# Kernel tuning notes

Measured on AMD Instinct MI355X. Metric: run time of the kernel, lower is better.

## Reference

```python
import jax, jax.numpy as jnp
import numpy as np

B, DIM, H, W = 512, 256, 14, 14
HEADS, KD, VD = 4, 16, 64  # key_dim=16, val_dim=attn_ratio*key_dim=64
RES = 14


def _bn(x, g, b, rm, rv, eps=1e-5):
    # eval-mode BatchNorm2d folded into per-channel affine
    s = g / jnp.sqrt(rv + eps)
    return x * s[None, :, None, None] + (b - rm * s)[None, :, None, None]


def setup_inputs() -> dict:
    key = jax.random.key(0)
    ks = jax.random.split(key, 6)
    # relative position bias index table: offset (|dy|,|dx|) -> flat index
    ii = np.arange(RES * RES)
    ry, rx = ii // RES, ii % RES
    dyo = np.abs(ry[:, None] - ry[None, :])
    dxo = np.abs(rx[:, None] - rx[None, :])
    bias_idxs = jnp.asarray(dyo * RES + dxo, dtype=jnp.int32)  # [196,196]
    QKV_OUT = 2 * KD + VD  # 96
    inp = {
        'x': jax.random.normal(ks[0], (B, DIM, H, W), jnp.float32),
        'qkv_w': jax.random.normal(ks[1], (HEADS, QKV_OUT, DIM // HEADS), jnp.float32) * 0.05,
        'qkv_g': jnp.ones((HEADS, QKV_OUT), jnp.float32),
        'qkv_b': jnp.zeros((HEADS, QKV_OUT), jnp.float32),
        'qkv_rm': jnp.zeros((HEADS, QKV_OUT), jnp.float32),
        'qkv_rv': jnp.ones((HEADS, QKV_OUT), jnp.float32),
        'dw_w': jax.random.normal(ks[2], (HEADS, KD, 1, 5, 5), jnp.float32) * 0.05,
        'dw_g': jnp.ones((HEADS, KD), jnp.float32),
        'dw_b': jnp.zeros((HEADS, KD), jnp.float32),
        'dw_rm': jnp.zeros((HEADS, KD), jnp.float32),
        'dw_rv': jnp.ones((HEADS, KD), jnp.float32),
        'proj_w': jax.random.normal(ks[3], (DIM, VD * HEADS), jnp.float32) * 0.05,
        'proj_g': jnp.ones((DIM,), jnp.float32),
        'proj_b': jnp.zeros((DIM,), jnp.float32),
        'proj_rm': jnp.zeros((DIM,), jnp.float32),
        'proj_rv': jnp.ones((DIM,), jnp.float32),
        'attn_biases': jax.random.normal(ks[4], (HEADS, RES * RES), jnp.float32) * 0.02,
        'bias_idxs': bias_idxs,
    }
    return inp


def reference(x, qkv_w, qkv_g, qkv_b, qkv_rm, qkv_rv,
              dw_w, dw_g, dw_b, dw_rm, dw_rv,
              proj_w, proj_g, proj_b, proj_rm, proj_rv,
              attn_biases, bias_idxs):
    Bc, C, Hc, Wc = x.shape
    N = Hc * Wc
    scale = KD ** -0.5
    bias = attn_biases[:, bias_idxs]  # [HEADS, N, N]
    chunks = jnp.split(x, HEADS, axis=1)  # per-head [B, dim//heads, H, W]
    feat = chunks[0]
    outs = []
    for h in range(HEADS):  # cascading residual -> inherently sequential over heads
        if h > 0:
            feat = feat + chunks[h]
        f = jnp.einsum('oc,bchw->bohw', qkv_w[h], feat)  # 1x1 conv
        f = _bn(f, qkv_g[h], qkv_b[h], qkv_rm[h], qkv_rv[h])
        q, k, v = f[:, :KD], f[:, KD:2 * KD], f[:, 2 * KD:]
        # 5x5 depthwise conv on q, padding 2
        q = jax.lax.conv_general_dilated(
            q, dw_w[h], window_strides=(1, 1), padding=[(2, 2), (2, 2)],
            dimension_numbers=('NCHW', 'OIHW', 'NCHW'), feature_group_count=KD)
        q = _bn(q, dw_g[h], dw_b[h], dw_rm[h], dw_rv[h])
        qf = q.reshape(Bc, KD, N) * scale
        kf = k.reshape(Bc, KD, N)
        vf = v.reshape(Bc, VD, N)
        attn = jnp.einsum('bdn,bdm->bnm', qf, kf) + bias[h]  # [B, N, N]
        attn = jax.nn.softmax(attn, axis=-1)
        feat = jnp.einsum('bdm,bnm->bdn', vf, attn).reshape(Bc, VD, Hc, Wc)
        outs.append(feat)
    y = jax.nn.relu(jnp.concatenate(outs, axis=1))  # [B, VD*HEADS, H, W]
    y = jnp.einsum('oc,bchw->bohw', proj_w, y)
    return _bn(y, proj_g, proj_b, proj_rm, proj_rv)
```

## Files before the change

### kernel.cpp

```cpp
#include <hip/hip_runtime.h>
#include <math.h>

#define BATCH 512
#define DIM 256
#define HEADS 4
#define KD 16
#define VD 64
#define NQ 196
#define CHW (DIM * NQ)

typedef __attribute__((ext_vector_type(8))) short short8;
typedef __attribute__((ext_vector_type(4))) float f32x4;

#define MFMA16(A, B, C) __builtin_amdgcn_mfma_f32_16x16x32_bf16((A), (B), (C), 0, 0, 0)

__device__ __forceinline__ unsigned short f2bf(float f) {
    unsigned int u = __float_as_uint(f);
    u += 0x7FFFu + ((u >> 16) & 1u);
    return (unsigned short)(u >> 16);
}
__device__ __forceinline__ float bf2f(unsigned short h) {
    return __uint_as_float(((unsigned int)h) << 16);
}

#define OFF_QC    0
#define OFF_P0    16640
#define OFF_P1    33280
#define OFF_QRAW  49920
#define OFF_KB1   63232
#define OFF_KB2   81152
#define OFF_VBH   99072
#define OFF_VBL   128768
#define OFF_DEN4  158464
#define OFF_SB    161792
#define OFF_TB    162176
#define OFF_DWS   162560
#define OFF_DWT   162624
#define SMEM_BYTES 162688

__global__ __launch_bounds__(256)
void prep_kernel(const float* __restrict__ attn_biases,
                 const int* __restrict__ bias_idxs,
                 const float* __restrict__ qkv_w,
                 const float* __restrict__ proj_w,
                 float* __restrict__ biasg,
                 unsigned short* __restrict__ whH,
                 unsigned short* __restrict__ whL,
                 unsigned short* __restrict__ pwH,
                 unsigned short* __restrict__ pwL) {
    int i = blockIdx.x * 256 + threadIdx.x;
    const int T1 = HEADS * NQ * NQ;
    const int T2 = HEADS * 96 * 64;
    const int T3 = DIM * DIM;
    if (i < T1) {
        int h = i / (NQ * NQ);
        int r = i - h * (NQ * NQ);
        biasg[i] = attn_biases[h * NQ + bias_idxs[r]];
    } else if (i < T1 + T2) {
        int j = i - T1;
        float v = qkv_w[j];
        unsigned short hh = f2bf(v);
        whH[j] = hh;
        whL[j] = f2bf(v - bf2f(hh));
    } else if (i < T1 + T2 + T3) {
        int j = i - T1 - T2;
        float v = proj_w[j];
        unsigned short hh = f2bf(v);
        pwH[j] = hh;
        pwL[j] = f2bf(v - bf2f(hh));
    }
}

__global__ __launch_bounds__(1024, 4)
void cascade_attn_kernel(const float* __restrict__ x,
                         const unsigned short* __restrict__ whH,
                         const unsigned short* __restrict__ whL,
                         const float* __restrict__ qkv_g,
                         const float* __restrict__ qkv_b,
                         const float* __restrict__ qkv_rm,
                         const float* __restrict__ qkv_rv,
                         const float* __restrict__ dw_w,
                         const float* __restrict__ dw_g,
                         const float* __restrict__ dw_b,
                         const float* __restrict__ dw_rm,
                         const float* __restrict__ dw_rv,
                         const float* __restrict__ biasg,
                         unsigned short* __restrict__ yrelu,
                         const unsigned short* __restrict__ pwH,
                         const unsigned short* __restrict__ pwL,
                         const float* __restrict__ pg,
                         const float* __restrict__ pb,
                         const float* __restrict__ prm,
                         const float* __restrict__ prv,
                         float* __restrict__ out) {
    extern __shared__ __align__(16) char smem[];
    unsigned short* featU = (unsigned short*)(smem + OFF_QC);
    unsigned short* qc    = (unsigned short*)(smem + OFF_QC);
    unsigned short* Pb0   = (unsigned short*)(smem + OFF_P0);
    unsigned short* Pb1   = (unsigned short*)(smem + OFF_P1);
    float*          qraw  = (float*)(smem + OFF_QRAW);
    unsigned short* kb1   = (unsigned short*)(smem + OFF_KB1);
    unsigned short* kb2   = (unsigned short*)(smem + OFF_KB2);
    unsigned short* vbH   = (unsigned short*)(smem + OFF_VBH);
    unsigned short* vbL   = (unsigned short*)(smem + OFF_VBL);
    float*          den4  = (float*)(smem + OFF_DEN4);
    float*          sbT   = (float*)(smem + OFF_SB);
    float*          tbT   = (float*)(smem + OFF_TB);
    float*          dwsT  = (float*)(smem + OFF_DWS);
    float*          dwtT  = (float*)(smem + OFF_DWT);

    const int b    = blockIdx.x;
    const int tid  = threadIdx.x;
    const int w    = tid >> 6;
    const int li   = tid & 15;
    const int quad = (tid >> 4) & 3;
    const int tn0  = tid % NQ;
    const int tc0  = tid / NQ;

    for (int t = tid; t < SMEM_BYTES / 4; t += 1024) ((unsigned int*)smem)[t] = 0u;
    __syncthreads();
    for (int t = tid; t < VD * NQ; t += 1024) {
        int n = t % NQ, c = t / NQ;
        featU[n * 72 + c] = f2bf(x[((size_t)b * DIM + c) * NQ + n]);
    }
    __syncthreads();

    for (int h = 0; h < HEADS; ++h) {
        if (tid < 96) {
            float s = qkv_g[h * 96 + tid] * rsqrtf(qkv_rv[h * 96 + tid] + 1e-5f);
            sbT[tid] = s;
            tbT[tid] = qkv_b[h * 96 + tid] - qkv_rm[h * 96 + tid] * s;
        } else if (tid < 112) {
            int c = tid - 96;
            float s = dw_g[h * 16 + c] * rsqrtf(dw_rv[h * 16 + c] + 1e-5f);
            dwsT[c] = s;
            dwtT[c] = dw_b[h * 16 + c] - dw_rm[h * 16 + c] * s;
        }
        __syncthreads();

        for (int T = w; T < 78; T += 16) {
            int ot = T / 13, nt = T - ot * 13;
            const size_t wb = ((size_t)h * 96 + ot * 16 + li) * 64;
            short8 ah0 = *(const short8*)(whH + wb + quad * 8);
            short8 al0 = *(const short8*)(whL + wb + quad * 8);
            short8 ah1 = *(const short8*)(whH + wb + 32 + quad * 8);
            short8 al1 = *(const short8*)(whL + wb + 32 + quad * 8);
            short8 b0 = *(const short8*)(featU + (nt * 16 + li) * 72 + quad * 8);
            short8 b1 = *(const short8*)(featU + (nt * 16 + li) * 72 + 32 + quad * 8);
            f32x4 acc = {0.f, 0.f, 0.f, 0.f};
            acc = MFMA16(ah0, b0, acc);
            acc = MFMA16(al0, b0, acc);
            acc = MFMA16(ah1, b1, acc);
            acc = MFMA16(al1, b1, acc);
            int n = nt * 16 + li;
            bool nok = (n < NQ);
            #pragma unroll
            for (int r = 0; r < 4; ++r) {
                int o = ot * 16 + quad * 4 + r;
                float val = acc[r] * sbT[o] + tbT[o];
                if (nok) {
                    if (o < 16) {
                        qraw[o * 208 + n] = val;
                    } else if (o < 32) {
                        int c = o - 16;
                        unsigned short hh = f2bf(val);
                        kb1[n * 40 + c] = hh;
                        kb1[n * 40 + 16 + c] = hh;
                        kb2[n * 40 + c] = f2bf(val - bf2f(hh));
                    } else {
                        int d = o - 32;
                        unsigned short hh = f2bf(val);
                        vbH[d * 232 + n] = hh;
                        vbL[d * 232 + n] = f2bf(val - bf2f(hh));
                    }
                }
            }
        }
        __syncthreads();

        {
            int n = tn0, c = tc0, py = tn0 / 14, px = tn0 - (tn0 / 14) * 14;
            for (int t = tid; t < KD * NQ; t += 1024) {
                const float* qr = qraw + c * 208;
                const float* wdc = dw_w + ((size_t)h * KD + c) * 25;
                float accv = 0.f;
                #pragma unroll
                for (int ky = 0; ky < 5; ++ky) {
                    int yy = py + ky - 2;
                    if (yy < 0 || yy >= 14) continue;
                    #pragma unroll
                    for (int kx = 0; kx < 5; ++kx) {
                        int xx = px + kx - 2;
                        if (xx < 0 || xx >= 14) continue;
                        accv = fmaf(wdc[ky * 5 + kx], qr[yy * 14 + xx], accv);
                    }
                }
                float val = fmaf(accv, dwsT[c], dwtT[c]) * 0.25f;
                unsigned short hh = f2bf(val);
                qc[n * 40 + c] = hh;
                qc[n * 40 + 16 + c] = f2bf(val - bf2f(hh));
                n += 44; c += 5; px += 2; py += 3;
                if (px >= 14) { px -= 14; ++py; }
                if (n >= NQ) { n -= NQ; ++c; py -= 14; }
            }
        }
        if (tid < 832) den4[tid] = 0.f;
        __syncthreads();

        f32x4 pacc[4];
        #pragma unroll
        for (int s = 0; s < 4; ++s) pacc[s] = (f32x4){0.f, 0.f, 0.f, 0.f};

        auto spass = [&](int mi2, unsigned short* __restrict__ PbW) {
            for (int T = w; T < 26; T += 16) {
                int s = (T >= 13) ? 1 : 0;
                int nt = T - s * 13;
                int n0 = nt * 16;
                int mg = mi2 * 32 + s * 16 + li;
                bool mok = (mg < NQ);
                float bias4[4];
                #pragma unroll
                for (int r = 0; r < 4; ++r) {
                    int n = n0 + quad * 4 + r;
                    int ni = n < NQ ? n : NQ - 1;
                    int mgi = mg < NQ ? mg : NQ - 1;
                    bias4[r] = biasg[(size_t)h * (NQ * NQ) + ni * NQ + mgi];
                }
                short8 q  = *(const short8*)(qc  + (n0 + li) * 40 + quad * 8);
                short8 k1 = *(const short8*)(kb1 + mg * 40 + quad * 8);
                short8 k2 = *(const short8*)(kb2 + mg * 40 + quad * 8);
                f32x4 acc = {0.f, 0.f, 0.f, 0.f};
                acc = MFMA16(q, k1, acc);
                acc = MFMA16(q, k2, acc);
                #pragma unroll
                for (int r = 0; r < 4; ++r) {
                    float e = mok ? __expf(acc[r] + bias4[r]) : 0.f;
                    PbW[(n0 + quad * 4 + r) * 40 + s * 16 + li] = f2bf(e);
                }
            }
        };

        spass(0, Pb0);
        __syncthreads();

        for (int mi = 0; mi < 7; ++mi) {
            unsigned short* PbR = (mi & 1) ? Pb1 : Pb0;
            unsigned short* PbW = (mi & 1) ? Pb0 : Pb1;
            if (mi < 6) spass(mi + 1, PbW);

            if (tid < 832) {
                int n = tid >> 2, part = tid & 3;
                short8 pv = *(const short8*)(PbR + n * 40 + part * 8);
                float sum = 0.f;
                #pragma unroll
                for (int j = 0; j < 8; ++j) sum += bf2f((unsigned short)pv[j]);
                den4[n * 4 + part] += sum;
            }
            #pragma unroll
            for (int slot = 0; slot < 4; ++slot) {
                int T = w + slot * 16;
                if (T < 52) {
                    int dt = T / 13, nt = T - dt * 13;
                    short8 p  = *(const short8*)(PbR + (nt * 16 + li) * 40 + quad * 8);
                    short8 vh = *(const short8*)(vbH + (dt * 16 + li) * 232 + mi * 32 + quad * 8);
                    short8 vl = *(const short8*)(vbL + (dt * 16 + li) * 232 + mi * 32 + quad * 8);
                    pacc[slot] = MFMA16(p, vh, pacc[slot]);
                    pacc[slot] = MFMA16(p, vl, pacc[slot]);
                }
            }
            __syncthreads();
        }

        #pragma unroll
        for (int slot = 0; slot < 4; ++slot) {
            int T = w + slot * 16;
            if (T < 52) {
                int dt = T / 13, nt = T - dt * 13;
                int d = dt * 16 + li;
                #pragma unroll
                for (int r = 0; r < 4; ++r) {
                    int n = nt * 16 + quad * 4 + r;
                    if (n < NQ) {
                        f32x4 dv = *(const f32x4*)(den4 + n * 4);
                        float dn = (dv.x + dv.y) + (dv.z + dv.w);
                        float val = pacc[slot][r] / dn;
                        featU[n * 72 + d] = f2bf(val);
                    }
                }
            }
        }
        __syncthreads();

        for (int t = tid; t < (VD * NQ) / 8; t += 1024) {
            int n  = t >> 3;
            int c0 = (t & 7) * 8;
            short8 u = *(const short8*)(featU + n * 72 + c0);
            short8 ru;
            #pragma unroll
            for (int j = 0; j < 8; ++j) {
                unsigned short uu = (unsigned short)u[j];
                ru[j] = (short)((uu & 0x8000u) ? (unsigned short)0 : uu);
            }
            *(short8*)(yrelu + ((size_t)b * NQ + n) * DIM + h * VD + c0) = ru;
        }
        __syncthreads();

        if (h < 3) {
            for (int t = tid; t < VD * NQ; t += 1024) {
                int n = t % NQ, c = t / NQ;
                float v = bf2f(featU[n * 72 + c]) + x[((size_t)b * DIM + (h + 1) * VD + c) * NQ + n];
                featU[n * 72 + c] = f2bf(v);
            }
            for (int t = tid; t < 12 * 64; t += 1024)
                featU[(NQ + t / 64) * 72 + (t & 63)] = 0;
        }
        __syncthreads();
    }

    {
        __threadfence_block();
        unsigned short* ych0 = Pb0;
        unsigned short* ych1 = Pb1;
        const int sn = tid >> 2;
        const int sc = (tid & 3) * 8;
        const unsigned short* ysrc = yrelu + ((size_t)b * NQ + sn) * DIM + sc;
        const short8 z8 = {0, 0, 0, 0, 0, 0, 0, 0};

        if (sn < NQ)       *(short8*)(ych0 + sn * 40 + sc) = *(const short8*)(ysrc);
        else if (sn < 208) *(short8*)(ych0 + sn * 40 + sc) = z8;
        __syncthreads();

        const int o0 = w * 16;
        const unsigned short* pHb = pwH + (size_t)(o0 + li) * 256 + quad * 8;
        const unsigned short* pLb = pwL + (size_t)(o0 + li) * 256 + quad * 8;

        f32x4 acc[13];
        #pragma unroll
        for (int nt = 0; nt < 13; ++nt) acc[nt] = (f32x4){0.f, 0.f, 0.f, 0.f};

        #pragma unroll
        for (int ks = 0; ks < 8; ++ks) {
            unsigned short* cur = (ks & 1) ? ych1 : ych0;
            unsigned short* nxt = (ks & 1) ? ych0 : ych1;
            short8 nv;
            if (ks < 7 && sn < NQ) nv = *(const short8*)(ysrc + (ks + 1) * 32);
            short8 ah = *(const short8*)(pHb + ks * 32);
            short8 al = *(const short8*)(pLb + ks * 32);
            #pragma unroll
            for (int nt = 0; nt < 13; ++nt) {
                short8 bx = *(const short8*)(cur + (nt * 16 + li) * 40 + quad * 8);
                acc[nt] = MFMA16(ah, bx, acc[nt]);
                acc[nt] = MFMA16(al, bx, acc[nt]);
            }
            if (ks < 7) {
                if (sn < NQ)       *(short8*)(nxt + sn * 40 + sc) = nv;
                else if (sn < 208) *(short8*)(nxt + sn * 40 + sc) = z8;
                __syncthreads();
            }
        }

        #pragma unroll
        for (int r = 0; r < 4; ++r) {
            int o = o0 + quad * 4 + r;
            float s = pg[o] * rsqrtf(prv[o] + 1e-5f);
            float t = pb[o] - prm[o] * s;
            #pragma unroll
            for (int nt = 0; nt < 13; ++nt) {
                int n = nt * 16 + li;
                if (n < NQ)
                    out[(size_t)b * CHW + (size_t)o * NQ + n] = fmaf(acc[nt][r], s, t);
            }
        }
    }
}

extern "C" void kernel_launch(void* const* d_in, const int* in_sizes, int n_in,
                              void* d_out, int out_size, void* d_ws, size_t ws_size,
                              hipStream_t stream) {
    const float* x        = (const float*)d_in[0];
    const float* qkv_w    = (const float*)d_in[1];
    const float* qkv_g    = (const float*)d_in[2];
    const float* qkv_b    = (const float*)d_in[3];
    const float* qkv_rm   = (const float*)d_in[4];
    const float* qkv_rv   = (const float*)d_in[5];
    const float* dw_w     = (const float*)d_in[6];
    const float* dw_g     = (const float*)d_in[7];
    const float* dw_b     = (const float*)d_in[8];
    const float* dw_rm    = (const float*)d_in[9];
    const float* dw_rv    = (const float*)d_in[10];
    const float* proj_w   = (const float*)d_in[11];
    const float* proj_g   = (const float*)d_in[12];
    const float* proj_b   = (const float*)d_in[13];
    const float* proj_rm  = (const float*)d_in[14];
    const float* proj_rv  = (const float*)d_in[15];
    const float* attn_bs  = (const float*)d_in[16];
    const int*   bias_idx = (const int*)d_in[17];

    char* ws = (char*)d_ws;
    float* biasg = (float*)ws;
    unsigned short* yrelu = (unsigned short*)(ws + 614656);
    unsigned short* whH = (unsigned short*)(ws + 51994880);
    unsigned short* whL = (unsigned short*)(ws + 52044032);
    unsigned short* pwH = (unsigned short*)(ws + 52093184);
    unsigned short* pwL = (unsigned short*)(ws + 52224256);

    {
        int total = HEADS * NQ * NQ + HEADS * 96 * 64 + DIM * DIM;
        hipLaunchKernelGGL(prep_kernel, dim3((total + 255) / 256), dim3(256),
                           0, stream, attn_bs, bias_idx, qkv_w, proj_w,
                           biasg, whH, whL, pwH, pwL);
    }
    hipLaunchKernelGGL(cascade_attn_kernel, dim3(BATCH), dim3(1024),
                       SMEM_BYTES, stream,
                       x, whH, whL, qkv_g, qkv_b, qkv_rm, qkv_rv,
                       dw_w, dw_g, dw_b, dw_rm, dw_rv, biasg, yrelu,
                       pwH, pwL, proj_g, proj_b, proj_rm, proj_rv,
                       (float*)d_out);
}
```

Measured before the change: 549.1 us.

## Accumulate projection per head in registers instead of round-tripping y through global

The projection GEMM is now split across heads. After each head's attention output is computed, its ReLU'd bf16 values are written into a shared-memory buffer (aliasing the K buffer), and the head's 64-channel slice of the projection is accumulated into per-wave register accumulators. This removes the global yrelu write and read-back and the final double-buffered projection loop. The cost is 13 extra f32x4 accumulators kept live across the whole head loop, which raises register pressure under the 1024-thread launch bounds. It also relies on the K buffer not being reused before the next head's sync.

```diff
diff --git a/kernel.cpp b/kernel.cpp
--- a/kernel.cpp
+++ b/kernel.cpp
@@ -85,7 +85,6 @@
                          const float* __restrict__ dw_rm,
                          const float* __restrict__ dw_rv,
                          const float* __restrict__ biasg,
-                         unsigned short* __restrict__ yrelu,
                          const unsigned short* __restrict__ pwH,
                          const unsigned short* __restrict__ pwL,
                          const float* __restrict__ pg,
@@ -108,6 +107,7 @@
     float*          tbT   = (float*)(smem + OFF_TB);
     float*          dwsT  = (float*)(smem + OFF_DWS);
     float*          dwtT  = (float*)(smem + OFF_DWT);
+    unsigned short* yrL   = (unsigned short*)(smem + OFF_KB1);
 
     const int b    = blockIdx.x;
     const int tid  = threadIdx.x;
@@ -116,6 +116,10 @@
     const int quad = (tid >> 4) & 3;
     const int tn0  = tid % NQ;
     const int tc0  = tid / NQ;
+
+    f32x4 prj[13];
+    #pragma unroll
+    for (int nt = 0; nt < 13; ++nt) prj[nt] = (f32x4){0.f, 0.f, 0.f, 0.f};
 
     for (int t = tid; t < SMEM_BYTES / 4; t += 1024) ((unsigned int*)smem)[t] = 0u;
     __syncthreads();
@@ -284,26 +288,30 @@
                         f32x4 dv = *(const f32x4*)(den4 + n * 4);
                         float dn = (dv.x + dv.y) + (dv.z + dv.w);
                         float val = pacc[slot][r] / dn;
-                        featU[n * 72 + d] = f2bf(val);
+                        unsigned short u = f2bf(val);
+                        featU[n * 72 + d] = u;
+                        yrL[n * 72 + d] = (u & 0x8000u) ? (unsigned short)0 : u;
                     }
                 }
             }
         }
         __syncthreads();
 
-        for (int t = tid; t < (VD * NQ) / 8; t += 1024) {
-            int n  = t >> 3;
-            int c0 = (t & 7) * 8;
-            short8 u = *(const short8*)(featU + n * 72 + c0);
-            short8 ru;
+        {
+            const int o0 = w * 16;
             #pragma unroll
-            for (int j = 0; j < 8; ++j) {
-                unsigned short uu = (unsigned short)u[j];
-                ru[j] = (short)((uu & 0x8000u) ? (unsigned short)0 : uu);
-            }
-            *(short8*)(yrelu + ((size_t)b * NQ + n) * DIM + h * VD + c0) = ru;
-        }
-        __syncthreads();
+            for (int ks2 = 0; ks2 < 2; ++ks2) {
+                const size_t wb2 = (size_t)(o0 + li) * 256 + h * 64 + ks2 * 32 + quad * 8;
+                short8 ah = *(const short8*)(pwH + wb2);
+                short8 al = *(const short8*)(pwL + wb2);
+                #pragma unroll
+                for (int nt = 0; nt < 13; ++nt) {
+                    short8 bx = *(const short8*)(yrL + (nt * 16 + li) * 72 + ks2 * 32 + quad * 8);
+                    prj[nt] = MFMA16(ah, bx, prj[nt]);
+                    prj[nt] = MFMA16(al, bx, prj[nt]);
+                }
+            }
+        }
 
         if (h < 3) {
             for (int t = tid; t < VD * NQ; t += 1024) {
@@ -318,47 +326,7 @@
     }
 
     {
-        __threadfence_block();
-        unsigned short* ych0 = Pb0;
-        unsigned short* ych1 = Pb1;
-        const int sn = tid >> 2;
-        const int sc = (tid & 3) * 8;
-        const unsigned short* ysrc = yrelu + ((size_t)b * NQ + sn) * DIM + sc;
-        const short8 z8 = {0, 0, 0, 0, 0, 0, 0, 0};
-
-        if (sn < NQ)       *(short8*)(ych0 + sn * 40 + sc) = *(const short8*)(ysrc);
-        else if (sn < 208) *(short8*)(ych0 + sn * 40 + sc) = z8;
-        __syncthreads();
-
         const int o0 = w * 16;
-        const unsigned short* pHb = pwH + (size_t)(o0 + li) * 256 + quad * 8;
-        const unsigned short* pLb = pwL + (size_t)(o0 + li) * 256 + quad * 8;
-
-        f32x4 acc[13];
-        #pragma unroll
-        for (int nt = 0; nt < 13; ++nt) acc[nt] = (f32x4){0.f, 0.f, 0.f, 0.f};
-
-        #pragma unroll
-        for (int ks = 0; ks < 8; ++ks) {
-            unsigned short* cur = (ks & 1) ? ych1 : ych0;
-            unsigned short* nxt = (ks & 1) ? ych0 : ych1;
-            short8 nv;
-            if (ks < 7 && sn < NQ) nv = *(const short8*)(ysrc + (ks + 1) * 32);
-            short8 ah = *(const short8*)(pHb + ks * 32);
-            short8 al = *(const short8*)(pLb + ks * 32);
-            #pragma unroll
-            for (int nt = 0; nt < 13; ++nt) {
-                short8 bx = *(const short8*)(cur + (nt * 16 + li) * 40 + quad * 8);
-                acc[nt] = MFMA16(ah, bx, acc[nt]);
-                acc[nt] = MFMA16(al, bx, acc[nt]);
-            }
-            if (ks < 7) {
-                if (sn < NQ)       *(short8*)(nxt + sn * 40 + sc) = nv;
-                else if (sn < 208) *(short8*)(nxt + sn * 40 + sc) = z8;
-                __syncthreads();
-            }
-        }
-
         #pragma unroll
         for (int r = 0; r < 4; ++r) {
             int o = o0 + quad * 4 + r;
@@ -368,7 +336,7 @@
             for (int nt = 0; nt < 13; ++nt) {
                 int n = nt * 16 + li;
                 if (n < NQ)
-                    out[(size_t)b * CHW + (size_t)o * NQ + n] = fmaf(acc[nt][r], s, t);
+                    out[(size_t)b * CHW + (size_t)o * NQ + n] = fmaf(prj[nt][r], s, t);
             }
         }
     }
@@ -398,11 +366,10 @@
 
     char* ws = (char*)d_ws;
     float* biasg = (float*)ws;
-    unsigned short* yrelu = (unsigned short*)(ws + 614656);
-    unsigned short* whH = (unsigned short*)(ws + 51994880);
-    unsigned short* whL = (unsigned short*)(ws + 52044032);
-    unsigned short* pwH = (unsigned short*)(ws + 52093184);
-    unsigned short* pwL = (unsigned short*)(ws + 52224256);
+    unsigned short* whH = (unsigned short*)(ws + 614656);
+    unsigned short* whL = (unsigned short*)(ws + 663808);
+    unsigned short* pwH = (unsigned short*)(ws + 712960);
+    unsigned short* pwL = (unsigned short*)(ws + 844032);
 
     {
         int total = HEADS * NQ * NQ + HEADS * 96 * 64 + DIM * DIM;
@@ -413,7 +380,7 @@
     hipLaunchKernelGGL(cascade_attn_kernel, dim3(BATCH), dim3(1024),
                        SMEM_BYTES, stream,
                        x, whH, whL, qkv_g, qkv_b, qkv_rm, qkv_rv,
-                       dw_w, dw_g, dw_b, dw_rm, dw_rv, biasg, yrelu,
+                       dw_w, dw_g, dw_b, dw_rm, dw_rv, biasg,
                        pwH, pwL, proj_g, proj_b, proj_rm, proj_rv,
                        (float*)d_out);
 }
```

After: 614.8 us. 1.12x slower.
